# Kernel tuning notes

Measured on AMD Instinct MI355X. Metric: run time of the kernel, lower is better.

The kernel has to match this reference:

```python
import jax, jax.numpy as jnp
from jax import lax
import numpy as np

B, D, P, C = 16384, 256, 512, 20  # batch, input_dim, prototype_dim, n_class


def setup_inputs() -> dict:
    key = jax.random.key(0)
    k1, k2, k3 = jax.random.split(key, 3)
    return {
        "inputs": jax.random.normal(k1, (B, D), dtype=jnp.float32),
        "W": jax.random.normal(k2, (P, D), dtype=jnp.float32),
        "BETA": jax.random.normal(k3, (P, C), dtype=jnp.float32),
        "alpha": jnp.zeros((P, 1), dtype=jnp.float32),
        "gamma": jnp.full((P, 1), 0.1, dtype=jnp.float32),
        "n_class": C,
        "prototype_dim": P,
    }


def reference(inputs, W, BETA, alpha, gamma, n_class, prototype_dim):
    # inputs: [B, D], W: [P, D], BETA: [P, C], alpha/gamma: [P, 1]
    BETA2 = BETA * BETA
    U = BETA2 / BETA2.sum(axis=1, keepdims=True)          # [P, C]
    alphap = 0.99 / (1.0 + jnp.exp(-alpha))               # [P, 1]
    # d[k, b] = 0.5 * ||x_b - W_k||^2 via the expanded quadratic form
    d = 0.5 * (jnp.sum(W * W, axis=1)[:, None]
               + jnp.sum(inputs * inputs, axis=1)[None, :]
               - 2.0 * W @ inputs.T)                      # [P, B]
    expo = jnp.exp(-(gamma * gamma) * d)                  # [P, B]
    s = alphap * expo                                     # [P, B]

    bsz = inputs.shape[0]

    def step(mk, xs):
        # mk: [C+1, B] combined mass; xs = (U_k [C], s_k [B])
        Uk, sk = xs
        m_c = Uk[:, None] * sk[None, :]                   # [C, B] singleton masses
        m_n = 1.0 - sk                                    # [B]   mass on ignorance
        mk_c, mk_n = mk[:-1], mk[-1]
        new_c = mk_c * (m_c + m_n[None, :]) + m_c * mk_n[None, :]
        new_n = mk_n * m_n
        return jnp.concatenate([new_c, new_n[None, :]], axis=0), None

    mk0 = jnp.concatenate([jnp.zeros((n_class, bsz), dtype=inputs.dtype),
                           jnp.ones((1, bsz), dtype=inputs.dtype)], axis=0)
    mk, _ = lax.scan(step, mk0, (U, s))                   # sequential over P prototypes
    K = mk.sum(axis=0)                                    # [B]
    return (mk / K[None, :]).T                            # [B, C+1]
```

## Files before the change

kernel.cpp:

```cpp
#include <hip/hip_runtime.h>
#include <math.h>


#define NBATCH 16384
#define ND     256
#define NP     512
#define NCLS   20
#define OC     21

typedef short  short8  __attribute__((ext_vector_type(8)));
typedef short  short4v __attribute__((ext_vector_type(4)));
typedef unsigned short ushort8 __attribute__((ext_vector_type(8)));
typedef float  f32x16  __attribute__((ext_vector_type(16)));

#define OFF_PWH 0u
#define OFF_PWL 262144u
#define OFF_VS  524288u
#define OFF_WQ  567296u
#define OFF_AP  569344u
#define OFF_G2  571392u
#define OFF_SG  1048576u
#define WS_BIG  ((size_t)(OFF_SG + 33554432u))

__device__ __forceinline__ unsigned short f2bf_rn(float f) {
  unsigned int u = __float_as_uint(f);
  unsigned int r = (u + 0x7FFFu + ((u >> 16) & 1u)) >> 16;
  return (unsigned short)r;
}
__device__ __forceinline__ float bf2f(unsigned short h) {
  return __uint_as_float(((unsigned int)h) << 16);
}

__global__ __launch_bounds__(256)
void prep(const float* __restrict__ Wsrc, const float* __restrict__ BETA,
          const float* __restrict__ alpha, const float* __restrict__ gamma,
          unsigned short* __restrict__ dh, unsigned short* __restrict__ dl,
          float* __restrict__ sq, float* __restrict__ VS,
          float* __restrict__ AP, float* __restrict__ G2)
{
  const int bid = blockIdx.x;
  if (bid < 64) {
    const int tid = bid * 256 + threadIdx.x;
    const int row = tid >> 5, seg = tid & 31;
    const float4* s4 = (const float4*)(Wsrc + (size_t)row * ND + seg * 8);
    const float4 a = s4[0], b = s4[1];
    const float v[8] = {a.x, a.y, a.z, a.w, b.x, b.y, b.z, b.w};
    ushort8 hv, lv;
    float ssq = 0.f;
    #pragma unroll
    for (int j = 0; j < 8; ++j) {
      ssq = fmaf(v[j], v[j], ssq);
      const unsigned short hh = f2bf_rn(v[j]);
      hv[j] = hh;
      lv[j] = f2bf_rn(v[j] - bf2f(hh));
    }
    const int tile = row >> 5, m = row & 31, step = seg >> 1, r = seg & 1;
    const size_t cidx = (size_t)(tile * 16 + step) * 64 + m + 32 * r;
    *(ushort8*)(dh + cidx * 8) = hv;
    *(ushort8*)(dl + cidx * 8) = lv;
    #pragma unroll
    for (int off = 1; off < 32; off <<= 1) ssq += __shfl_xor(ssq, off, 64);
    if (seg == 0) sq[row] = ssq;
  } else {
    const int k = (bid - 64) * 256 + threadIdx.x;
    if (k >= NP) return;
    float bv[NCLS], bs = 0.f;
    #pragma unroll
    for (int c = 0; c < NCLS; ++c) { bv[c] = BETA[k * NCLS + c]; bs = fmaf(bv[c], bv[c], bs); }
    const float binv = 1.f / bs;
    #pragma unroll
    for (int c = 0; c < NCLS; ++c) VS[c * NP + k] = 1.f - bv[c] * bv[c] * binv;
    VS[NCLS * NP + k] = 1.f;
    AP[k] = 0.99f / (1.f + __expf(-alpha[k]));
    const float g = gamma[k];
    G2[k] = g * g;
  }
}

__global__ __launch_bounds__(512)
void gemm_s(const float* __restrict__ X,
            const unsigned short* __restrict__ PWH, const unsigned short* __restrict__ PWL,
            const float* __restrict__ WQ, const float* __restrict__ AP,
            const float* __restrict__ G2, float* __restrict__ SG)
{
  __shared__ __align__(16) short Ah[16384], Al[16384];
  __shared__ float xqs[64];

  const int t    = threadIdx.x;
  const int lane = t & 63;
  const int wv   = __builtin_amdgcn_readfirstlane(t >> 6);
  const int tile = blockIdx.x;
  const int bbase = tile * 64;
  const int pl = lane & 31, h = lane >> 5;

  {
    const int r  = t >> 3;
    const int sg = t & 7;
    const int rsh = r >> 5, rm = r & 31;
    const float* xrow = X + (size_t)(bbase + r) * ND;
    float ssq = 0.f;
    #pragma unroll
    for (int it = 0; it < 8; ++it) {
      const int c0 = it * 32 + sg * 4;
      const float4 v = *(const float4*)(xrow + c0);
      const float vv[4] = {v.x, v.y, v.z, v.w};
      short4v h4, l4;
      #pragma unroll
      for (int j = 0; j < 4; ++j) {
        ssq = fmaf(vv[j], vv[j], ssq);
        const unsigned short hh = f2bf_rn(vv[j]);
        h4[j] = (short)hh;
        l4[j] = (short)f2bf_rn(vv[j] - bf2f(hh));
      }
      const int step = c0 >> 4, half = (c0 >> 3) & 1, j0 = c0 & 7;
      const int base = (((rsh * 16 + step) * 64) + (rm + 32 * half)) * 8 + j0;
      *(short4v*)&Ah[base] = h4;
      *(short4v*)&Al[base] = l4;
    }
    ssq += __shfl_xor(ssq, 1, 64);
    ssq += __shfl_xor(ssq, 2, 64);
    ssq += __shfl_xor(ssq, 4, 64);
    if (sg == 0) xqs[r] = ssq;
  }
  __syncthreads();

  #pragma unroll 1
  for (int chunk = 0; chunk < 2; ++chunk) {
    const int kp = chunk * 256 + wv * 32 + pl;
    const float wqk = WQ[kp], apk = AP[kp], g2k = G2[kp];
    const short8* bHc = (const short8*)PWH + (size_t)(chunk * 8 + wv) * 1024 + lane;
    const short8* bLc = (const short8*)PWL + (size_t)(chunk * 8 + wv) * 1024 + lane;

    #pragma unroll 1
    for (int sh = 0; sh < 2; ++sh) {
      short8 wbh[4], wbl[4];
      #pragma unroll
      for (int p = 0; p < 4; ++p) { wbh[p] = bHc[p * 64]; wbl[p] = bLc[p * 64]; }

      f32x16 accA, accB, accC;
      #pragma unroll
      for (int i = 0; i < 16; ++i) { accA[i] = 0.f; accB[i] = 0.f; accC[i] = 0.f; }
      const short8* aH = (const short8*)Ah + (size_t)sh * 1024 + lane;
      const short8* aL = (const short8*)Al + (size_t)sh * 1024 + lane;
      #pragma unroll
      for (int step = 0; step < 16; ++step) {
        const short8 ah = aH[step * 64], al = aL[step * 64];
        const short8 bh = wbh[step & 3], bl = wbl[step & 3];
        if (step < 12) {
          wbh[step & 3] = bHc[(step + 4) * 64];
          wbl[step & 3] = bLc[(step + 4) * 64];
        }
        accA = __builtin_amdgcn_mfma_f32_32x32x16_bf16(ah, bh, accA, 0, 0, 0);
        accB = __builtin_amdgcn_mfma_f32_32x32x16_bf16(ah, bl, accB, 0, 0, 0);
        accC = __builtin_amdgcn_mfma_f32_32x32x16_bf16(al, bh, accC, 0, 0, 0);
      }

      float* sgb = SG + (size_t)(tile * 2 + sh) * 16384 + kp;
      #pragma unroll
      for (int rg = 0; rg < 16; ++rg) {
        const int   m  = (rg & 3) + 8 * (rg >> 2) + 4 * h;
        const float dv = 0.5f * (wqk + xqs[sh * 32 + m])
                       - (accA[rg] + accB[rg] + accC[rg]);
        sgb[m * 512] = apk * __expf(-g2k * dv);
      }
    }
  }
}

__global__ __launch_bounds__(512)
void combine(const float* __restrict__ SG, const float* __restrict__ VS,
             float* __restrict__ OUT)
{
  __shared__ float S[12160];

  const int t    = threadIdx.x;
  const int lane = t & 63;
  const int wv   = __builtin_amdgcn_readfirstlane(t >> 6);
  const int tile = blockIdx.x;
  const int k0   = wv * 64;

  const float* srow = SG + ((size_t)(tile * 2 + (lane >> 5)) * 16384)
                         + (size_t)(lane & 31) * 512 + k0;
  float sv[64];
  #pragma unroll
  for (int q = 0; q < 16; ++q)
    *(float4*)&sv[4 * q] = *(const float4*)(srow + 4 * q);

  float Apc[OC];
  const float* vt = VS + k0;
  for (int c = 0; c < OC; ++c) {
    const float* vp = vt + (size_t)c * NP;
    float f[64];
    #pragma unroll
    for (int j = 0; j < 64; ++j) f[j] = fmaf(-sv[j], vp[j], 1.0f);
    #pragma unroll
    for (int w = 32; w >= 1; w >>= 1)
      for (int j = 0; j < w; ++j) f[j] *= f[j + w];
    Apc[c] = f[0];
  }

  #pragma unroll
  for (int c = 0; c < OC; ++c) S[(wv * OC + c) * 64 + lane] = Apc[c];
  __syncthreads();
  float* R = S + 10752;
  {
    const int b = t & 63, j = t >> 6;
    for (int c = j; c < OC; c += 8) {
      float p = S[c * 64 + b];
      #pragma unroll
      for (int w = 1; w < 8; ++w) p *= S[(w * OC + c) * 64 + b];
      R[c * 64 + b] = p;
    }
  }
  __syncthreads();
  float* kv = R + 1344;
  if (t < 64) {
    const float Nv = R[NCLS * 64 + t];
    float K = Nv;
    #pragma unroll
    for (int c = 0; c < NCLS; ++c) K += R[c * 64 + t] - Nv;
    kv[t] = 1.0f / K;
  }
  __syncthreads();
  for (int idx = t; idx < 64 * OC; idx += 512) {
    const int b = idx / OC, c = idx - b * OC;
    const float Nv = R[NCLS * 64 + b];
    OUT[(size_t)tile * 64 * OC + idx] =
        ((c < NCLS) ? (R[c * 64 + b] - Nv) : Nv) * kv[b];
  }
}

__global__ __launch_bounds__(512)
void evid_main(const float* __restrict__ X,
               const unsigned short* __restrict__ PWH, const unsigned short* __restrict__ PWL,
               const float* __restrict__ VS, const float* __restrict__ WQ,
               const float* __restrict__ AP, const float* __restrict__ G2,
               float* __restrict__ OUT)
{
  __shared__ __align__(16) short Ah[16384], Al[16384];
  __shared__ __align__(16) float sst[2][8192];
  __shared__ float xqs[64];

  const int t    = threadIdx.x;
  const int lane = t & 63;
  const int wv   = __builtin_amdgcn_readfirstlane(t >> 6);
  const int tile = blockIdx.x;
  const int bbase = tile * 64;
  const int sh = wv & 1, pg = wv >> 1;
  const int pl = lane & 31, h = lane >> 5;

  const short8* bH = (const short8*)PWH + (size_t)pg * 1024 + lane;
  const short8* bL = (const short8*)PWL + (size_t)pg * 1024 + lane;
  short8 wbh[4], wbl[4];
  #pragma unroll
  for (int p = 0; p < 4; ++p) { wbh[p] = bH[p * 64]; wbl[p] = bL[p * 64]; }

  {
    const int r  = t >> 3;
    const int sg = t & 7;
    const int rsh = r >> 5, rm = r & 31;
    const float* xrow = X + (size_t)(bbase + r) * ND;
    float ssq = 0.f;
    #pragma unroll
    for (int it = 0; it < 8; ++it) {
      const int c0 = it * 32 + sg * 4;
      const float4 v = *(const float4*)(xrow + c0);
      const float vv[4] = {v.x, v.y, v.z, v.w};
      short4v h4, l4;
      #pragma unroll
      for (int j = 0; j < 4; ++j) {
        ssq = fmaf(vv[j], vv[j], ssq);
        const unsigned short hh = f2bf_rn(vv[j]);
        h4[j] = (short)hh;
        l4[j] = (short)f2bf_rn(vv[j] - bf2f(hh));
      }
      const int step = c0 >> 4, half = (c0 >> 3) & 1, j0 = c0 & 7;
      const int base = (((rsh * 16 + step) * 64) + (rm + 32 * half)) * 8 + j0;
      *(short4v*)&Ah[base] = h4;
      *(short4v*)&Al[base] = l4;
    }
    ssq += __shfl_xor(ssq, 1, 64);
    ssq += __shfl_xor(ssq, 2, 64);
    ssq += __shfl_xor(ssq, 4, 64);
    if (sg == 0) xqs[r] = ssq;
  }
  __syncthreads();

  float xqv[16];
  #pragma unroll
  for (int rg = 0; rg < 16; ++rg)
    xqv[rg] = xqs[sh * 32 + (rg & 3) + 8 * (rg >> 2) + 4 * h];

  float Apc[OC];
  #pragma unroll
  for (int c = 0; c < OC; ++c) Apc[c] = 1.0f;

  #pragma unroll 1
  for (int chunk = 0; chunk < 4; ++chunk) {
    const int par = chunk & 1;
    float* sp = &sst[par][0];
    const int kp = chunk * 128 + pg * 32 + pl;
    const float wqk = WQ[kp], apk = AP[kp], g2k = G2[kp];

    f32x16 accA, accB, accC;
    #pragma unroll
    for (int i = 0; i < 16; ++i) { accA[i] = 0.f; accB[i] = 0.f; accC[i] = 0.f; }
    const short8* aH = (const short8*)Ah + (size_t)sh * 1024 + lane;
    const short8* aL = (const short8*)Al + (size_t)sh * 1024 + lane;
    #pragma unroll
    for (int step = 0; step < 16; ++step) {
      const short8 ah = aH[step * 64], al = aL[step * 64];
      const short8 bh = wbh[step & 3], bl = wbl[step & 3];
      if (step < 12) {
        wbh[step & 3] = bH[(step + 4) * 64];
        wbl[step & 3] = bL[(step + 4) * 64];
      }
      accA = __builtin_amdgcn_mfma_f32_32x32x16_bf16(ah, bh, accA, 0, 0, 0);
      accB = __builtin_amdgcn_mfma_f32_32x32x16_bf16(ah, bl, accB, 0, 0, 0);
      accC = __builtin_amdgcn_mfma_f32_32x32x16_bf16(al, bh, accC, 0, 0, 0);
    }

    #pragma unroll
    for (int rg = 0; rg < 16; ++rg) {
      const int   m  = (rg & 3) + 8 * (rg >> 2) + 4 * h;
      const int   b  = sh * 32 + m;
      const int   col = (pg * 32 + pl + 4 * m) & 127;
      const float dv = 0.5f * (wqk + xqv[rg]) - (accA[rg] + accB[rg] + accC[rg]);
      sp[b * 128 + col] = apk * __expf(-g2k * dv);
    }

    if (chunk < 3) {
      bH += 4096; bL += 4096;
      #pragma unroll
      for (int p = 0; p < 4; ++p) { wbh[p] = bH[p * 64]; wbl[p] = bL[p * 64]; }
    }

    __syncthreads();

    {
      const int kl = wv * 16;
      float sv[16];
      #pragma unroll
      for (int q = 0; q < 4; ++q) {
        const int col = (kl + 4 * (lane & 31) + 4 * q) & 127;
        *(float4*)&sv[4 * q] = *(const float4*)&sp[lane * 128 + col];
      }
      const float* vtab = VS + chunk * 128 + kl;
      for (int c = 0; c < OC; ++c) {
        const float* vp = vtab + (size_t)c * NP;
        float f[16];
        #pragma unroll
        for (int j = 0; j < 16; ++j) f[j] = fmaf(-sv[j], vp[j], 1.0f);
        const float p0 = (f[0] * f[1]) * (f[2] * f[3]);
        const float p1 = (f[4] * f[5]) * (f[6] * f[7]);
        const float p2 = (f[8] * f[9]) * (f[10] * f[11]);
        const float p3 = (f[12] * f[13]) * (f[14] * f[15]);
        Apc[c] *= (p0 * p1) * (p2 * p3);
      }
    }
  }

  __syncthreads();
  float* S = &sst[0][0];
  #pragma unroll
  for (int c = 0; c < OC; ++c) S[(wv * OC + c) * 64 + lane] = Apc[c];
  __syncthreads();
  float* R  = S + 11008;
  {
    const int b = t & 63, j = t >> 6;
    for (int c = j; c < OC; c += 8) {
      float p = S[c * 64 + b];
      #pragma unroll
      for (int w = 1; w < 8; ++w) p *= S[(w * OC + c) * 64 + b];
      R[c * 64 + b] = p;
    }
  }
  __syncthreads();
  float* kv = R + 1344;
  if (t < 64) {
    const float Nv = R[NCLS * 64 + t];
    float K = Nv;
    #pragma unroll
    for (int c = 0; c < NCLS; ++c) K += R[c * 64 + t] - Nv;
    kv[t] = 1.0f / K;
  }
  __syncthreads();
  for (int idx = t; idx < 64 * OC; idx += 512) {
    const int b = idx / OC, c = idx - b * OC;
    const float Nv = R[NCLS * 64 + b];
    const float ik = kv[b];
    OUT[(size_t)tile * 64 * OC + idx] = (c < NCLS) ? (R[c * 64 + b] - Nv) * ik : Nv * ik;
  }
}

extern "C" void kernel_launch(void* const* d_in, const int* in_sizes, int n_in,
                              void* d_out, int out_size, void* d_ws, size_t ws_size,
                              hipStream_t stream) {
  (void)in_sizes; (void)n_in; (void)out_size;
  const float* X     = (const float*)d_in[0];
  const float* Wm    = (const float*)d_in[1];
  const float* BETA  = (const float*)d_in[2];
  const float* ALPHA = (const float*)d_in[3];
  const float* GAMMA = (const float*)d_in[4];
  float* OUT = (float*)d_out;

  char* ws = (char*)d_ws;
  unsigned short* PWH = (unsigned short*)(ws + OFF_PWH);
  unsigned short* PWL = (unsigned short*)(ws + OFF_PWL);
  float* VS = (float*)(ws + OFF_VS);
  float* WQ = (float*)(ws + OFF_WQ);
  float* AP = (float*)(ws + OFF_AP);
  float* G2 = (float*)(ws + OFF_G2);

  hipLaunchKernelGGL(prep, dim3(66), dim3(256), 0, stream,
                     Wm, BETA, ALPHA, GAMMA, PWH, PWL, WQ, VS, AP, G2);

  if (ws_size >= WS_BIG) {
    float* SG = (float*)(ws + OFF_SG);
    hipLaunchKernelGGL(gemm_s, dim3(NBATCH/64), dim3(512), 0, stream,
                       X, PWH, PWL, WQ, AP, G2, SG);
    hipLaunchKernelGGL(combine, dim3(NBATCH/64), dim3(512), 0, stream,
                       SG, VS, OUT);
  } else {
    hipLaunchKernelGGL(evid_main, dim3(NBATCH/64), dim3(512), 0, stream,
                       X, PWH, PWL, VS, WQ, AP, G2, OUT);
  }
}
```

Baseline: 106.4 us.

## Fuse GEMM with per-half product combine, drop 32MB intermediate buffer

Replaces the gemm_s + combine pair with a gemm_comb kernel that splits each 64-row tile across two blocks, one per half of the prototypes. Each block computes its s values, stages them in LDS with a skewed layout, and reduces the per-class products locally. It writes only small partial products, and a light finish kernel multiplies the two halves and normalises. This removes the 32MB global round-trip of the s matrix and doubles the grid for more parallelism. The cost is extra LDS syncs and the A-tile bf16 conversion being done twice per tile.

```diff
diff --git a/kernel.cpp b/kernel.cpp
--- a/kernel.cpp
+++ b/kernel.cpp
@@ -19,8 +19,8 @@
 #define OFF_WQ  567296u
 #define OFF_AP  569344u
 #define OFF_G2  571392u
-#define OFF_SG  1048576u
-#define WS_BIG  ((size_t)(OFF_SG + 33554432u))
+#define OFF_PP  1048576u
+#define WS_BIG  ((size_t)(OFF_PP + 2752512u))
 
 __device__ __forceinline__ unsigned short f2bf_rn(float f) {
   unsigned int u = __float_as_uint(f);
@@ -77,19 +77,61 @@
   }
 }
 
+__device__ __forceinline__ void mfma_pass(
+    const short* __restrict__ Ah, const short* __restrict__ Al,
+    const short8* __restrict__ bHc, const short8* __restrict__ bLc,
+    const int lane, const int sh, const float* __restrict__ xqs,
+    const float wqk, const float apk, const float g2k, float* __restrict__ sout)
+{
+  short8 wbh[4], wbl[4];
+  #pragma unroll
+  for (int p = 0; p < 4; ++p) { wbh[p] = bHc[p * 64]; wbl[p] = bLc[p * 64]; }
+
+  f32x16 accA, accB, accC;
+  #pragma unroll
+  for (int i = 0; i < 16; ++i) { accA[i] = 0.f; accB[i] = 0.f; accC[i] = 0.f; }
+  const short8* aH = (const short8*)Ah + (size_t)sh * 1024 + lane;
+  const short8* aL = (const short8*)Al + (size_t)sh * 1024 + lane;
+  #pragma unroll
+  for (int step = 0; step < 16; ++step) {
+    const short8 ah = aH[step * 64], al = aL[step * 64];
+    const short8 bh = wbh[step & 3], bl = wbl[step & 3];
+    if (step < 12) {
+      wbh[step & 3] = bHc[(step + 4) * 64];
+      wbl[step & 3] = bLc[(step + 4) * 64];
+    }
+    accA = __builtin_amdgcn_mfma_f32_32x32x16_bf16(ah, bh, accA, 0, 0, 0);
+    accB = __builtin_amdgcn_mfma_f32_32x32x16_bf16(ah, bl, accB, 0, 0, 0);
+    accC = __builtin_amdgcn_mfma_f32_32x32x16_bf16(al, bh, accC, 0, 0, 0);
+  }
+  const int h = lane >> 5;
+  #pragma unroll
+  for (int rg = 0; rg < 16; ++rg) {
+    const int   m  = (rg & 3) + 8 * (rg >> 2) + 4 * h;
+    const float dv = 0.5f * (wqk + xqs[sh * 32 + m])
+                   - (accA[rg] + accB[rg] + accC[rg]);
+    sout[rg] = apk * __expf(-g2k * dv);
+  }
+}
+
 __global__ __launch_bounds__(512)
-void gemm_s(const float* __restrict__ X,
-            const unsigned short* __restrict__ PWH, const unsigned short* __restrict__ PWL,
-            const float* __restrict__ WQ, const float* __restrict__ AP,
-            const float* __restrict__ G2, float* __restrict__ SG)
+void gemm_comb(const float* __restrict__ X,
+               const unsigned short* __restrict__ PWH, const unsigned short* __restrict__ PWL,
+               const float* __restrict__ VS, const float* __restrict__ WQ,
+               const float* __restrict__ AP, const float* __restrict__ G2,
+               float* __restrict__ PP)
 {
-  __shared__ __align__(16) short Ah[16384], Al[16384];
+  __shared__ __align__(16) char pool[65536];
   __shared__ float xqs[64];
+  short* Ah = (short*)pool;
+  short* Al = (short*)(pool + 32768);
+  float* sc = (float*)pool;
 
   const int t    = threadIdx.x;
   const int lane = t & 63;
   const int wv   = __builtin_amdgcn_readfirstlane(t >> 6);
-  const int tile = blockIdx.x;
+  const int bx   = blockIdx.x;
+  const int tile = bx >> 1, half = bx & 1;
   const int bbase = tile * 64;
   const int pl = lane & 31, h = lane >> 5;
 
@@ -112,8 +154,8 @@
         h4[j] = (short)hh;
         l4[j] = (short)f2bf_rn(vv[j] - bf2f(hh));
       }
-      const int step = c0 >> 4, half = (c0 >> 3) & 1, j0 = c0 & 7;
-      const int base = (((rsh * 16 + step) * 64) + (rm + 32 * half)) * 8 + j0;
+      const int step = c0 >> 4, hf = (c0 >> 3) & 1, j0 = c0 & 7;
+      const int base = (((rsh * 16 + step) * 64) + (rm + 32 * hf)) * 8 + j0;
       *(short4v*)&Ah[base] = h4;
       *(short4v*)&Al[base] = l4;
     }
@@ -124,110 +166,87 @@
   }
   __syncthreads();
 
-  #pragma unroll 1
-  for (int chunk = 0; chunk < 2; ++chunk) {
-    const int kp = chunk * 256 + wv * 32 + pl;
-    const float wqk = WQ[kp], apk = AP[kp], g2k = G2[kp];
-    const short8* bHc = (const short8*)PWH + (size_t)(chunk * 8 + wv) * 1024 + lane;
-    const short8* bLc = (const short8*)PWL + (size_t)(chunk * 8 + wv) * 1024 + lane;
-
-    #pragma unroll 1
-    for (int sh = 0; sh < 2; ++sh) {
-      short8 wbh[4], wbl[4];
-      #pragma unroll
-      for (int p = 0; p < 4; ++p) { wbh[p] = bHc[p * 64]; wbl[p] = bLc[p * 64]; }
-
-      f32x16 accA, accB, accC;
-      #pragma unroll
-      for (int i = 0; i < 16; ++i) { accA[i] = 0.f; accB[i] = 0.f; accC[i] = 0.f; }
-      const short8* aH = (const short8*)Ah + (size_t)sh * 1024 + lane;
-      const short8* aL = (const short8*)Al + (size_t)sh * 1024 + lane;
-      #pragma unroll
-      for (int step = 0; step < 16; ++step) {
-        const short8 ah = aH[step * 64], al = aL[step * 64];
-        const short8 bh = wbh[step & 3], bl = wbl[step & 3];
-        if (step < 12) {
-          wbh[step & 3] = bHc[(step + 4) * 64];
-          wbl[step & 3] = bLc[(step + 4) * 64];
-        }
-        accA = __builtin_amdgcn_mfma_f32_32x32x16_bf16(ah, bh, accA, 0, 0, 0);
-        accB = __builtin_amdgcn_mfma_f32_32x32x16_bf16(ah, bl, accB, 0, 0, 0);
-        accC = __builtin_amdgcn_mfma_f32_32x32x16_bf16(al, bh, accC, 0, 0, 0);
-      }
-
-      float* sgb = SG + (size_t)(tile * 2 + sh) * 16384 + kp;
-      #pragma unroll
-      for (int rg = 0; rg < 16; ++rg) {
-        const int   m  = (rg & 3) + 8 * (rg >> 2) + 4 * h;
-        const float dv = 0.5f * (wqk + xqs[sh * 32 + m])
-                       - (accA[rg] + accB[rg] + accC[rg]);
-        sgb[m * 512] = apk * __expf(-g2k * dv);
-      }
-    }
-  }
-}
-
-__global__ __launch_bounds__(512)
-void combine(const float* __restrict__ SG, const float* __restrict__ VS,
-             float* __restrict__ OUT)
+  const int kp = half * 256 + wv * 32 + pl;
+  const float wqk = WQ[kp], apk = AP[kp], g2k = G2[kp];
+  const short8* bHc = (const short8*)PWH + (size_t)(half * 8 + wv) * 1024 + lane;
+  const short8* bLc = (const short8*)PWL + (size_t)(half * 8 + wv) * 1024 + lane;
+
+  float sreg0[16], sreg1[16];
+  mfma_pass(Ah, Al, bHc, bLc, lane, 0, xqs, wqk, apk, g2k, sreg0);
+  mfma_pass(Ah, Al, bHc, bLc, lane, 1, xqs, wqk, apk, g2k, sreg1);
+
+  __syncthreads();
+
+  {
+    const int p = wv * 32 + pl;
+    #pragma unroll
+    for (int rg = 0; rg < 16; ++rg) {
+      const int m  = (rg & 3) + 8 * (rg >> 2) + 4 * h;
+      sc[m * 256 + ((p + 4 * m) & 255)] = sreg0[rg];
+      const int b1 = m + 32;
+      sc[b1 * 256 + ((p + 4 * b1) & 255)] = sreg1[rg];
+    }
+  }
+  __syncthreads();
+
+  float Apc[OC];
+  {
+    const int j3 = wv;
+    float sv[32];
+    const int c0 = (j3 * 32 + 4 * lane);
+    #pragma unroll
+    for (int q = 0; q < 8; ++q)
+      *(float4*)&sv[4 * q] = *(const float4*)&sc[lane * 256 + ((c0 + 4 * q) & 255)];
+
+    const float* vt = VS + half * 256 + j3 * 32;
+    for (int c = 0; c < OC; ++c) {
+      const float* vp = vt + (size_t)c * NP;
+      float f8[8];
+      #pragma unroll
+      for (int j = 0; j < 8; ++j) f8[j] = fmaf(-sv[j], vp[j], 1.0f);
+      #pragma unroll
+      for (int j = 8; j < 32; ++j) f8[j & 7] *= fmaf(-sv[j], vp[j], 1.0f);
+      Apc[c] = ((f8[0] * f8[1]) * (f8[2] * f8[3])) *
+               ((f8[4] * f8[5]) * (f8[6] * f8[7]));
+    }
+  }
+  __syncthreads();
+
+  float* E = (float*)pool;
+  #pragma unroll
+  for (int c = 0; c < OC; ++c) E[(wv * OC + c) * 64 + lane] = Apc[c];
+  __syncthreads();
+  {
+    const int b = t & 63, j = t >> 6;
+    float* pp = PP + (size_t)bx * (OC * 64);
+    for (int c = j; c < OC; c += 8) {
+      float p = E[c * 64 + b];
+      #pragma unroll
+      for (int w = 1; w < 8; ++w) p *= E[(w * OC + c) * 64 + b];
+      pp[c * 64 + b] = p;
+    }
+  }
+}
+
+__global__ __launch_bounds__(256)
+void finish(const float* __restrict__ PP, float* __restrict__ OUT)
 {
-  __shared__ float S[12160];
-
-  const int t    = threadIdx.x;
-  const int lane = t & 63;
-  const int wv   = __builtin_amdgcn_readfirstlane(t >> 6);
-  const int tile = blockIdx.x;
-  const int k0   = wv * 64;
-
-  const float* srow = SG + ((size_t)(tile * 2 + (lane >> 5)) * 16384)
-                         + (size_t)(lane & 31) * 512 + k0;
-  float sv[64];
-  #pragma unroll
-  for (int q = 0; q < 16; ++q)
-    *(float4*)&sv[4 * q] = *(const float4*)(srow + 4 * q);
-
-  float Apc[OC];
-  const float* vt = VS + k0;
-  for (int c = 0; c < OC; ++c) {
-    const float* vp = vt + (size_t)c * NP;
-    float f[64];
-    #pragma unroll
-    for (int j = 0; j < 64; ++j) f[j] = fmaf(-sv[j], vp[j], 1.0f);
-    #pragma unroll
-    for (int w = 32; w >= 1; w >>= 1)
-      for (int j = 0; j < w; ++j) f[j] *= f[j + w];
-    Apc[c] = f[0];
-  }
-
-  #pragma unroll
-  for (int c = 0; c < OC; ++c) S[(wv * OC + c) * 64 + lane] = Apc[c];
-  __syncthreads();
-  float* R = S + 10752;
-  {
-    const int b = t & 63, j = t >> 6;
-    for (int c = j; c < OC; c += 8) {
-      float p = S[c * 64 + b];
-      #pragma unroll
-      for (int w = 1; w < 8; ++w) p *= S[(w * OC + c) * 64 + b];
-      R[c * 64 + b] = p;
-    }
-  }
-  __syncthreads();
-  float* kv = R + 1344;
-  if (t < 64) {
-    const float Nv = R[NCLS * 64 + t];
-    float K = Nv;
-    #pragma unroll
-    for (int c = 0; c < NCLS; ++c) K += R[c * 64 + t] - Nv;
-    kv[t] = 1.0f / K;
-  }
-  __syncthreads();
-  for (int idx = t; idx < 64 * OC; idx += 512) {
-    const int b = idx / OC, c = idx - b * OC;
-    const float Nv = R[NCLS * 64 + b];
-    OUT[(size_t)tile * 64 * OC + idx] =
-        ((c < NCLS) ? (R[c * 64 + b] - Nv) : Nv) * kv[b];
-  }
+  const int s = blockIdx.x * 256 + threadIdx.x;
+  const int tile = s >> 6, b = s & 63;
+  const float* p0 = PP + (size_t)tile * (2 * OC * 64) + b;
+  const float* p1 = p0 + OC * 64;
+  float A[OC];
+  #pragma unroll
+  for (int c = 0; c < OC; ++c) A[c] = p0[c * 64] * p1[c * 64];
+  const float Nv = A[NCLS];
+  float K = Nv;
+  #pragma unroll
+  for (int c = 0; c < NCLS; ++c) K += A[c] - Nv;
+  const float ik = 1.0f / K;
+  float* o = OUT + (size_t)s * OC;
+  #pragma unroll
+  for (int c = 0; c < NCLS; ++c) o[c] = (A[c] - Nv) * ik;
+  o[NCLS] = Nv * ik;
 }
 
 __global__ __launch_bounds__(512)
@@ -274,8 +293,8 @@
         h4[j] = (short)hh;
         l4[j] = (short)f2bf_rn(vv[j] - bf2f(hh));
       }
-      const int step = c0 >> 4, half = (c0 >> 3) & 1, j0 = c0 & 7;
-      const int base = (((rsh * 16 + step) * 64) + (rm + 32 * half)) * 8 + j0;
+      const int step = c0 >> 4, hf = (c0 >> 3) & 1, j0 = c0 & 7;
+      const int base = (((rsh * 16 + step) * 64) + (rm + 32 * hf)) * 8 + j0;
       *(short4v*)&Ah[base] = h4;
       *(short4v*)&Al[base] = l4;
     }
@@ -416,11 +435,11 @@
                      Wm, BETA, ALPHA, GAMMA, PWH, PWL, WQ, VS, AP, G2);
 
   if (ws_size >= WS_BIG) {
-    float* SG = (float*)(ws + OFF_SG);
-    hipLaunchKernelGGL(gemm_s, dim3(NBATCH/64), dim3(512), 0, stream,
-                       X, PWH, PWL, WQ, AP, G2, SG);
-    hipLaunchKernelGGL(combine, dim3(NBATCH/64), dim3(512), 0, stream,
-                       SG, VS, OUT);
+    float* PP = (float*)(ws + OFF_PP);
+    hipLaunchKernelGGL(gemm_comb, dim3(NBATCH/32), dim3(512), 0, stream,
+                       X, PWH, PWL, VS, WQ, AP, G2, PP);
+    hipLaunchKernelGGL(finish, dim3(NBATCH/256), dim3(256), 0, stream,
+                       PP, OUT);
   } else {
     hipLaunchKernelGGL(evid_main, dim3(NBATCH/64), dim3(512), 0, stream,
                        X, PWH, PWL, VS, WQ, AP, G2, OUT);
```

After: 111.0 us. 4.4% more time.
